# Kernel tuning notes

Hardware: AMD Instinct MI355X
Metric: run time of the kernel (lower is better)

Reference implementation:

```python
import jax, jax.numpy as jnp
import numpy as np

C = 64  # num_features

def setup_inputs() -> dict:
    key = jax.random.key(0)
    k = jax.random.split(key, 5)
    B, H, W = 4, 512, 512
    s = 1.0 / np.sqrt(C)
    return {
        "features": jax.random.normal(k[0], (B, C, H, W), jnp.float32),
        "w_ih": jax.random.uniform(k[1], (3 * C, 3 * C), jnp.float32, -s, s),
        "w_hh": jax.random.uniform(k[2], (3 * C, C), jnp.float32, -s, s),
        "b_ih": jax.random.uniform(k[3], (3 * C,), jnp.float32, -s, s),
        "b_hh": jax.random.uniform(k[4], (3 * C,), jnp.float32, -s, s),
    }

def _gru_cell(x, h, w_ih, w_hh, b_ih, b_hh):
    # PyTorch GRUCell: gates ordered [reset, update, new]
    gi = x @ w_ih.T + b_ih
    gh = h @ w_hh.T + b_hh
    i_r, i_z, i_n = jnp.split(gi, 3, axis=-1)
    h_r, h_z, h_n = jnp.split(gh, 3, axis=-1)
    r = jax.nn.sigmoid(i_r + h_r)
    z = jax.nn.sigmoid(i_z + h_z)
    n = jnp.tanh(i_n + r * h_n)
    return (1.0 - z) * n + z * h

def reference(features, w_ih, w_hh, b_ih, b_hh):
    B, Cf, H, W = features.shape
    # move scan axis (W) to front: [W, B, H, C]
    f = jnp.transpose(features, (3, 0, 2, 1))
    pad = jnp.zeros((B, 1, Cf), features.dtype)

    def step(prev_col, cur_col):
        # prev_col: already-updated column d-1, [B, H, C]
        nb = jnp.concatenate([pad, prev_col, pad], axis=1)  # [B, H+2, C]
        x = jnp.concatenate([nb[:, :-2], nb[:, 1:-1], nb[:, 2:]], axis=-1)  # [B, H, 3C]
        new = _gru_cell(x.reshape(B * H, 3 * Cf), cur_col.reshape(B * H, Cf),
                        w_ih, w_hh, b_ih, b_hh).reshape(B, H, Cf)
        return new, new

    col0 = f[0]
    _, outs = jax.lax.scan(step, col0, f[1:])
    all_cols = jnp.concatenate([col0[None], outs], axis=0)  # [W, B, H, C]
    return jnp.transpose(all_cols, (1, 3, 2, 0))  # [B, C, H, W]
```

## Files before the change

### kernel.cpp

```cpp
#include <hip/hip_runtime.h>

typedef short short8 __attribute__((ext_vector_type(8)));
typedef float f32x4 __attribute__((ext_vector_type(4)));
typedef unsigned short u16;
typedef unsigned int u32;

#define C64 64
#define HWp (512*512)
#define NWG 256
#define PR 72
#define SLOTS 18
#define SBUF 2048
#define UBUF 2048
#define NEP 128

struct Ws {
  int flags[NWG][32];
  u32 haloT[NWG][2][4*64];
  u32 haloB[NWG][2][4*64];
};

__device__ __forceinline__ u16 f2bf(float f){
  u32 r;
  asm("v_cvt_pk_bf16_f32 %0, %1, %1" : "=v"(r) : "v"(f));
  return (u16)r;
}
__device__ __forceinline__ float bf2f(u16 h){ return __uint_as_float(((u32)h) << 16); }
__device__ __forceinline__ f32x4 splat4(float x){ f32x4 v = {x,x,x,x}; return v; }
__device__ __forceinline__ float sigm(float x){ return 1.f/(1.f + __expf(-x)); }
__device__ __forceinline__ float tanh_(float x){ float e = __expf(2.f*x); return 1.f - 2.f/(e + 1.f); }

#define MFMA16(a,b,c) __builtin_amdgcn_mfma_f32_16x16x32_bf16(a,b,c,0,0,0)
#define ATOM_ST(p,v) __hip_atomic_store((p),(v),__ATOMIC_RELAXED,__HIP_MEMORY_SCOPE_AGENT)
#define ATOM_LD(p)   __hip_atomic_load((p),__ATOMIC_RELAXED,__HIP_MEMORY_SCOPE_AGENT)
#define DOT3(acc, XH, XL, WH, WL) \
  acc = MFMA16(XH, WH, acc); acc = MFMA16(XL, WH, acc); acc = MFMA16(XH, WL, acc);

__global__ void reset_flags(int* flags) {
  if (threadIdx.x < NWG) flags[threadIdx.x * 32] = -1;
}

#define AKK(kk) {                                                        \
  const int _o = PS + aoff + ((kk)>>1)*PR + ((kk)&1)*32;                 \
  short8 Ah = *(const short8*)&sh[_o];                                   \
  short8 Al = *(const short8*)&sl[_o];                                   \
  DOT3(aR, Ah, Al, BihH[0][kk], BihL[0][kk]);                            \
  DOT3(aZ, Ah, Al, BihH[1][kk], BihL[1][kk]);                            \
  DOT3(aI, Ah, Al, BihH[2][kk], BihL[2][kk]); }

#define XKT(kt) {                                                        \
  const int _o = PU + aoff + (kt)*32;                                    \
  short8 Xh = *(const short8*)&uh[_o];                                   \
  short8 Xl = *(const short8*)&ul[_o];                                   \
  DOT3(aR, Xh, Xl, BhhH[0][kt], BhhL[0][kt]);                            \
  DOT3(aZ, Xh, Xl, BhhH[1][kt], BhhL[1][kt]);                            \
  DOT3(aH, Xh, Xl, BhhH[2][kt], BhhL[2][kt]); }

#define GWB(j) {                                                         \
  const int m = kgrp*4 + (j);                                            \
  const int absr = a - 4 + m;                                            \
  float r = sigm(aR[j]);                                                 \
  float z = sigm(aZ[j]);                                                 \
  float nn = tanh_(aI[j] + r*aH[j]);                                     \
  float cur = bf2f(uh[PU + m*PR + ch]) + bf2f(ul[PU + m*PR + ch]);       \
  float v = (1.f - z)*nn + z*cur;                                        \
  if ((unsigned)absr < 512u) {                                           \
    u16 h_ = f2bf(v);                                                    \
    sh[PN + (m+1)*PR + ch] = h_;                                         \
    sl[PN + (m+1)*PR + ch] = f2bf(v - bf2f(h_));                         \
  }                                                                      \
  if (m >= 4 && m < 12) ost[((m-4)*64 + ch)*16 + dc0 + DD] = f2bf(v);    \
  if (DD == 3) {                                                         \
    if (kgrp == 1) ATOM_ST(&ws->haloT[g][e&1][(j)*64 + ch], __float_as_uint(v)); \
    if (kgrp == 2) ATOM_ST(&ws->haloB[g][e&1][(j)*64 + ch], __float_as_uint(v)); \
  } }

#define UST(i) {                                                         \
  float v = cv[DD][i];                                                   \
  u16 h_ = f2bf(v);                                                      \
  uh[PV + uoff[i]] = h_;                                                 \
  ul[PV + uoff[i]] = f2bf(v - bf2f(h_));                                 \
  cv[DD][i] = nv[i]; }

#define STEP(DD_) {                                                      \
  enum { DD = DD_, PS = (DD&1)*SBUF, PN = ((DD&1)^1)*SBUF,               \
         PU = (DD&1)*UBUF, PV = ((DD&1)^1)*UBUF };                       \
  float nv[4];                                                           \
  { int cc = 4*e + 6 + DD; if (cc > 511) cc = 511;                       \
    nv[0] = fval0 ? frow0[cc] : 0.f;                                     \
    nv[1] = fval1 ? frow1[cc] : 0.f;                                     \
    nv[2] = fval2 ? frow2[cc] : 0.f;                                     \
    nv[3] = fval3 ? frow3[cc] : 0.f; }                                   \
  f32x4 aR = splat4(biasR), aZ = splat4(biasZ);                          \
  f32x4 aI = splat4(biasI), aH = splat4(biasHn);                         \
  AKK(0) AKK(1) AKK(2) AKK(3) AKK(4) AKK(5)                              \
  XKT(0) XKT(1)                                                          \
  GWB(0) GWB(1) GWB(2) GWB(3)                                            \
  UST(0) UST(1) UST(2) UST(3)                                            \
}

__global__ __launch_bounds__(256, 1)
void gru_scan(const float* __restrict__ feat,
              const float* __restrict__ w_ih,
              const float* __restrict__ w_hh,
              const float* __restrict__ b_ih,
              const float* __restrict__ b_hh,
              float* __restrict__ out,
              Ws* __restrict__ ws)
{
  __shared__ __align__(16) u16 sh[2*SBUF], sl[2*SBUF];
  __shared__ __align__(16) u16 uh[2*UBUF], ul[2*UBUF];
  __shared__ __align__(16) u16 ost[8*64*16];

  const int tid  = threadIdx.x;
  const int wgid = blockIdx.x;
  const int g    = (wgid & 7) * 32 + (wgid >> 3);
  const int b    = g >> 6;
  const int kband= g & 63;
  const int a    = kband * 8;
  const int lane = tid & 63;
  const int wid  = tid >> 6;
  const int ln16 = lane & 15;
  const int kgrp = lane >> 4;
  const int ch   = wid*16 + ln16;

  short8 BihH[3][6], BihL[3][6], BhhH[3][2], BhhL[3][2];
#pragma unroll
  for (int gg = 0; gg < 3; ++gg) {
    const int n = gg*64 + ch;
#pragma unroll
    for (int kk = 0; kk < 6; ++kk) {
      short8 vh, vl;
#pragma unroll
      for (int j = 0; j < 8; ++j) {
        float wv = w_ih[n*192 + kk*32 + kgrp*8 + j];
        u16 h = f2bf(wv); vh[j] = (short)h; vl[j] = (short)f2bf(wv - bf2f(h));
      }
      BihH[gg][kk] = vh; BihL[gg][kk] = vl;
    }
#pragma unroll
    for (int kt = 0; kt < 2; ++kt) {
      short8 vh, vl;
#pragma unroll
      for (int j = 0; j < 8; ++j) {
        float wv = w_hh[n*64 + kt*32 + kgrp*8 + j];
        u16 h = f2bf(wv); vh[j] = (short)h; vl[j] = (short)f2bf(wv - bf2f(h));
      }
      BhhH[gg][kt] = vh; BhhL[gg][kt] = vl;
    }
  }
  const float biasR  = b_ih[ch]       + b_hh[ch];
  const float biasZ  = b_ih[64 + ch]  + b_hh[64 + ch];
  const float biasI  = b_ih[128 + ch];
  const float biasHn = b_hh[128 + ch];

  const int aoff = ln16*PR + kgrp*8;
  const int lch  = tid & 63;
  const int lr0  = wid * 4;
  int uoff[4];
#pragma unroll
  for (int i = 0; i < 4; ++i) uoff[i] = (lr0 + i)*PR + lch;

  const float* fbase = feat + (size_t)(b*C64 + lch)*HWp;
  int ar0 = a - 4 + lr0;
  const bool fval0 = (unsigned)(ar0+0) < 512u;
  const bool fval1 = (unsigned)(ar0+1) < 512u;
  const bool fval2 = (unsigned)(ar0+2) < 512u;
  const bool fval3 = (unsigned)(ar0+3) < 512u;
  const float* frow0 = fbase + (size_t)(fval0 ? ar0+0 : 0)*512;
  const float* frow1 = fbase + (size_t)(fval1 ? ar0+1 : 0)*512;
  const float* frow2 = fbase + (size_t)(fval2 ? ar0+2 : 0)*512;
  const float* frow3 = fbase + (size_t)(fval3 ? ar0+3 : 0)*512;

  for (int i = tid; i < 2*SBUF; i += 256) { sh[i] = 0; sl[i] = 0; }
  for (int i = tid; i < 2*UBUF; i += 256) { uh[i] = 0; ul[i] = 0; }
  __syncthreads();
#pragma unroll
  for (int i = 0; i < 5; ++i) {
    const int s = wid + 4*i;
    if (s < SLOTS) {
      const int absr = a - 5 + s;
      if ((unsigned)absr < 512u) {
        float v = fbase[(size_t)absr*512];
        u16 h_ = f2bf(v);
        sh[s*PR + lch] = h_;
        sl[s*PR + lch] = f2bf(v - bf2f(h_));
        if (s >= 5 && s <= 12) out[(size_t)(b*C64 + lch)*HWp + (size_t)absr*512] = v;
      }
    }
  }
  float cv[4][4];
#pragma unroll
  for (int i = 0; i < 4; ++i) {
    const int absr = a - 4 + lr0 + i;
    const bool val = (unsigned)absr < 512u;
    const float* fr = fbase + (size_t)(val ? absr : 0)*512;
    float v1 = val ? fr[1] : 0.f;
    u16 h_ = f2bf(v1);
    uh[uoff[i]] = h_;
    ul[uoff[i]] = f2bf(v1 - bf2f(h_));
    cv[0][i] = val ? fr[2] : 0.f;
    cv[1][i] = val ? fr[3] : 0.f;
    cv[2][i] = val ? fr[4] : 0.f;
    cv[3][i] = val ? fr[5] : 0.f;
  }
  __syncthreads();

#pragma unroll 1
  for (int e = 0; e < NEP; ++e) {
    const int dc0 = (e & 3) * 4;
    STEP(0)
    __syncthreads();
    STEP(1)
    __syncthreads();
    STEP(2)
    if (e < NEP-1) {
      __syncthreads();
      STEP(3)
    }

    asm volatile("s_waitcnt vmcnt(0)" ::: "memory");
    __syncthreads();
    if (e < NEP-1 && tid == 0) ATOM_ST(&ws->flags[g][0], e);

    if (wid == 0 || wid == 3) {
      if ((e & 3) == 3) {
        const int t128  = (wid == 0) ? lane : 64 + lane;
        const int wbase = 4*(e-3) + 1;
#pragma unroll
        for (int i = 0; i < 4; ++i) {
          const int pi  = t128 + 128*i;
          const int row = pi >> 6, c = pi & 63;
          float* go = out + (size_t)(b*C64 + c)*HWp + (size_t)(a + row)*512 + wbase;
#pragma unroll
          for (int dc = 0; dc < 16; ++dc)
            if (wbase + dc <= 511) go[dc] = bf2f(ost[pi*16 + dc]);
        }
      }
    } else if (e < NEP-1) {
      if (wid == 1 && kband > 0) {
        int f = -1, guard = 0;
        while (f < e && ++guard < (1<<17)) {
          if (lane == 0) f = ATOM_LD(&ws->flags[g-1][0]);
          f = __shfl(f, 0);
          if (f < e) __builtin_amdgcn_s_sleep(1);
        }
        asm volatile("" ::: "memory");
#pragma unroll
        for (int i = 0; i < 4; ++i) {
          float v = __uint_as_float(ATOM_LD(&ws->haloB[g-1][e&1][i*64 + lane]));
          u16 h_ = f2bf(v);
          sh[(1+i)*PR + lane] = h_;
          sl[(1+i)*PR + lane] = f2bf(v - bf2f(h_));
        }
      }
      if (wid == 2 && kband < 63) {
        int f = -1, guard = 0;
        while (f < e && ++guard < (1<<17)) {
          if (lane == 0) f = ATOM_LD(&ws->flags[g+1][0]);
          f = __shfl(f, 0);
          if (f < e) __builtin_amdgcn_s_sleep(1);
        }
        asm volatile("" ::: "memory");
#pragma unroll
        for (int i = 0; i < 4; ++i) {
          float v = __uint_as_float(ATOM_LD(&ws->haloT[g+1][e&1][i*64 + lane]));
          u16 h_ = f2bf(v);
          sh[(13+i)*PR + lane] = h_;
          sl[(13+i)*PR + lane] = f2bf(v - bf2f(h_));
        }
      }
    }
    __syncthreads();
  }
}

extern "C" void kernel_launch(void* const* d_in, const int* in_sizes, int n_in,
                              void* d_out, int out_size, void* d_ws, size_t ws_size,
                              hipStream_t stream) {
  const float* feat = (const float*)d_in[0];
  const float* wih  = (const float*)d_in[1];
  const float* whh  = (const float*)d_in[2];
  const float* bih  = (const float*)d_in[3];
  const float* bhh  = (const float*)d_in[4];
  float* out = (float*)d_out;
  Ws* ws = (Ws*)d_ws;

  reset_flags<<<1, NWG, 0, stream>>>((int*)ws->flags);
  gru_scan<<<NWG, 256, 0, stream>>>(feat, wih, whh, bih, bhh, out, ws);
}
```

Measured before the change: 1.278 ms.

## Split MFMA accumulator chains, batch feature prefetch, and remap cur-column ownership

Each gate's MFMA accumulation now runs as two independent chains that are summed at the end, which shortens the dependent MFMA latency chain. Feature loads for the next four columns are now issued once per epoch as vector loads instead of scalar loads inside each step. Lanes are remapped so the thread that writes the current-column values into LDS also holds them in a register for the gate update, removing the LDS reads of cur. The output staging buffer is transposed to column-major, which changes LDS bank patterns on write and readback. The cost is more accumulator registers and a larger live register set under a one-block-per-CU launch bound.

After: 1.420 ms. 11.1% more time.

```diff
diff --git a/kernel.cpp b/kernel.cpp
--- a/kernel.cpp
+++ b/kernel.cpp
@@ -2,6 +2,7 @@
 
 typedef short short8 __attribute__((ext_vector_type(8)));
 typedef float f32x4 __attribute__((ext_vector_type(4)));
+typedef float f32x2 __attribute__((ext_vector_type(2)));
 typedef unsigned short u16;
 typedef unsigned int u32;
 
@@ -40,36 +41,36 @@
   if (threadIdx.x < NWG) flags[threadIdx.x * 32] = -1;
 }
 
-#define AKK(kk) {                                                        \
+#define AKK(S, kk) {                                                     \
   const int _o = PS + aoff + ((kk)>>1)*PR + ((kk)&1)*32;                 \
   short8 Ah = *(const short8*)&sh[_o];                                   \
   short8 Al = *(const short8*)&sl[_o];                                   \
-  DOT3(aR, Ah, Al, BihH[0][kk], BihL[0][kk]);                            \
-  DOT3(aZ, Ah, Al, BihH[1][kk], BihL[1][kk]);                            \
-  DOT3(aI, Ah, Al, BihH[2][kk], BihL[2][kk]); }
-
-#define XKT(kt) {                                                        \
+  DOT3(aR##S, Ah, Al, BihH[0][kk], BihL[0][kk]);                         \
+  DOT3(aZ##S, Ah, Al, BihH[1][kk], BihL[1][kk]);                         \
+  DOT3(aI##S, Ah, Al, BihH[2][kk], BihL[2][kk]); }
+
+#define XKT(S, kt) {                                                     \
   const int _o = PU + aoff + (kt)*32;                                    \
   short8 Xh = *(const short8*)&uh[_o];                                   \
   short8 Xl = *(const short8*)&ul[_o];                                   \
-  DOT3(aR, Xh, Xl, BhhH[0][kt], BhhL[0][kt]);                            \
-  DOT3(aZ, Xh, Xl, BhhH[1][kt], BhhL[1][kt]);                            \
-  DOT3(aH, Xh, Xl, BhhH[2][kt], BhhL[2][kt]); }
+  DOT3(aR##S, Xh, Xl, BhhH[0][kt], BhhL[0][kt]);                         \
+  DOT3(aZ##S, Xh, Xl, BhhH[1][kt], BhhL[1][kt]);                         \
+  DOT3(aH##S, Xh, Xl, BhhH[2][kt], BhhL[2][kt]); }
 
 #define GWB(j) {                                                         \
   const int m = kgrp*4 + (j);                                            \
   const int absr = a - 4 + m;                                            \
-  float r = sigm(aR[j]);                                                 \
-  float z = sigm(aZ[j]);                                                 \
-  float nn = tanh_(aI[j] + r*aH[j]);                                     \
-  float cur = bf2f(uh[PU + m*PR + ch]) + bf2f(ul[PU + m*PR + ch]);       \
-  float v = (1.f - z)*nn + z*cur;                                        \
+  float r = sigm(aR0[j] + aR1[j]);                                       \
+  float z = sigm(aZ0[j] + aZ1[j]);                                       \
+  float nn = tanh_(aI0[j] + aI1[j] + r*(aH0[j] + aH1[j]));               \
+  float v = (1.f - z)*nn + z*cur[j];                                     \
   if ((unsigned)absr < 512u) {                                           \
     u16 h_ = f2bf(v);                                                    \
     sh[PN + (m+1)*PR + ch] = h_;                                         \
     sl[PN + (m+1)*PR + ch] = f2bf(v - bf2f(h_));                         \
   }                                                                      \
-  if (m >= 4 && m < 12) ost[((m-4)*64 + ch)*16 + dc0 + DD] = f2bf(v);    \
+  if (m >= 4 && m < 12)                                                  \
+    ost[(dc0 + DD)*512 + (m-4)*64 + ch] = f2bf(v);                       \
   if (DD == 3) {                                                         \
     if (kgrp == 1) ATOM_ST(&ws->haloT[g][e&1][(j)*64 + ch], __float_as_uint(v)); \
     if (kgrp == 2) ATOM_ST(&ws->haloB[g][e&1][(j)*64 + ch], __float_as_uint(v)); \
@@ -77,24 +78,21 @@
 
 #define UST(i) {                                                         \
   float v = cv[DD][i];                                                   \
+  cur[i] = v;                                                            \
   u16 h_ = f2bf(v);                                                      \
   uh[PV + uoff[i]] = h_;                                                 \
   ul[PV + uoff[i]] = f2bf(v - bf2f(h_));                                 \
-  cv[DD][i] = nv[i]; }
+  cv[DD][i] = nv4[i][DD]; }
 
 #define STEP(DD_) {                                                      \
   enum { DD = DD_, PS = (DD&1)*SBUF, PN = ((DD&1)^1)*SBUF,               \
          PU = (DD&1)*UBUF, PV = ((DD&1)^1)*UBUF };                       \
-  float nv[4];                                                           \
-  { int cc = 4*e + 6 + DD; if (cc > 511) cc = 511;                       \
-    nv[0] = fval0 ? frow0[cc] : 0.f;                                     \
-    nv[1] = fval1 ? frow1[cc] : 0.f;                                     \
-    nv[2] = fval2 ? frow2[cc] : 0.f;                                     \
-    nv[3] = fval3 ? frow3[cc] : 0.f; }                                   \
-  f32x4 aR = splat4(biasR), aZ = splat4(biasZ);                          \
-  f32x4 aI = splat4(biasI), aH = splat4(biasHn);                         \
-  AKK(0) AKK(1) AKK(2) AKK(3) AKK(4) AKK(5)                              \
-  XKT(0) XKT(1)                                                          \
+  f32x4 aR0 = splat4(biasR), aZ0 = splat4(biasZ);                        \
+  f32x4 aI0 = splat4(biasI), aH0 = splat4(biasHn);                       \
+  f32x4 aR1 = splat4(0.f), aZ1 = splat4(0.f);                            \
+  f32x4 aI1 = splat4(0.f), aH1 = splat4(0.f);                            \
+  AKK(0,0) AKK(1,3) AKK(0,1) AKK(1,4) AKK(0,2) AKK(1,5)                  \
+  XKT(0,0) XKT(1,1)                                                      \
   GWB(0) GWB(1) GWB(2) GWB(3)                                            \
   UST(0) UST(1) UST(2) UST(3)                                            \
 }
@@ -110,7 +108,7 @@
 {
   __shared__ __align__(16) u16 sh[2*SBUF], sl[2*SBUF];
   __shared__ __align__(16) u16 uh[2*UBUF], ul[2*UBUF];
-  __shared__ __align__(16) u16 ost[8*64*16];
+  __shared__ __align__(16) u16 ost[16*512];
 
   const int tid  = threadIdx.x;
   const int wgid = blockIdx.x;
@@ -155,60 +153,83 @@
   const float biasHn = b_hh[128 + ch];
 
   const int aoff = ln16*PR + kgrp*8;
-  const int lch  = tid & 63;
-  const int lr0  = wid * 4;
+  const int lrow = kgrp * 4;
   int uoff[4];
 #pragma unroll
-  for (int i = 0; i < 4; ++i) uoff[i] = (lr0 + i)*PR + lch;
-
-  const float* fbase = feat + (size_t)(b*C64 + lch)*HWp;
-  int ar0 = a - 4 + lr0;
-  const bool fval0 = (unsigned)(ar0+0) < 512u;
-  const bool fval1 = (unsigned)(ar0+1) < 512u;
-  const bool fval2 = (unsigned)(ar0+2) < 512u;
-  const bool fval3 = (unsigned)(ar0+3) < 512u;
-  const float* frow0 = fbase + (size_t)(fval0 ? ar0+0 : 0)*512;
-  const float* frow1 = fbase + (size_t)(fval1 ? ar0+1 : 0)*512;
-  const float* frow2 = fbase + (size_t)(fval2 ? ar0+2 : 0)*512;
-  const float* frow3 = fbase + (size_t)(fval3 ? ar0+3 : 0)*512;
+  for (int i = 0; i < 4; ++i) uoff[i] = (lrow + i)*PR + ch;
+
+  const float* fbase = feat + (size_t)(b*C64 + ch)*HWp;
+  const int ar0 = a - 4 + lrow;
+  bool fv[4];
+  const float* frw[4];
+#pragma unroll
+  for (int i = 0; i < 4; ++i) {
+    fv[i]  = (unsigned)(ar0 + i) < 512u;
+    frw[i] = fbase + (size_t)(fv[i] ? ar0 + i : 0)*512;
+  }
 
   for (int i = tid; i < 2*SBUF; i += 256) { sh[i] = 0; sl[i] = 0; }
   for (int i = tid; i < 2*UBUF; i += 256) { uh[i] = 0; ul[i] = 0; }
   __syncthreads();
-#pragma unroll
-  for (int i = 0; i < 5; ++i) {
-    const int s = wid + 4*i;
-    if (s < SLOTS) {
-      const int absr = a - 5 + s;
-      if ((unsigned)absr < 512u) {
-        float v = fbase[(size_t)absr*512];
-        u16 h_ = f2bf(v);
-        sh[s*PR + lch] = h_;
-        sl[s*PR + lch] = f2bf(v - bf2f(h_));
-        if (s >= 5 && s <= 12) out[(size_t)(b*C64 + lch)*HWp + (size_t)absr*512] = v;
-      }
-    }
-  }
-  float cv[4][4];
+  {
+    const int c0 = tid & 63;
+    const float* f0 = feat + (size_t)(b*C64 + c0)*HWp;
+#pragma unroll
+    for (int i = 0; i < 5; ++i) {
+      const int s = wid + 4*i;
+      if (s < SLOTS) {
+        const int absr = a - 5 + s;
+        if ((unsigned)absr < 512u) {
+          float v = f0[(size_t)absr*512];
+          u16 h_ = f2bf(v);
+          sh[s*PR + c0] = h_;
+          sl[s*PR + c0] = f2bf(v - bf2f(h_));
+          if (s >= 5 && s <= 12) out[(size_t)(b*C64 + c0)*HWp + (size_t)absr*512] = v;
+        }
+      }
+    }
+  }
+  float cv[4][4], cur[4], nv4[4][4];
 #pragma unroll
   for (int i = 0; i < 4; ++i) {
-    const int absr = a - 4 + lr0 + i;
-    const bool val = (unsigned)absr < 512u;
-    const float* fr = fbase + (size_t)(val ? absr : 0)*512;
-    float v1 = val ? fr[1] : 0.f;
+    float v1 = fv[i] ? frw[i][1] : 0.f;
     u16 h_ = f2bf(v1);
     uh[uoff[i]] = h_;
     ul[uoff[i]] = f2bf(v1 - bf2f(h_));
-    cv[0][i] = val ? fr[2] : 0.f;
-    cv[1][i] = val ? fr[3] : 0.f;
-    cv[2][i] = val ? fr[4] : 0.f;
-    cv[3][i] = val ? fr[5] : 0.f;
+    cur[i]   = v1;
+    cv[0][i] = fv[i] ? frw[i][2] : 0.f;
+    cv[1][i] = fv[i] ? frw[i][3] : 0.f;
+    cv[2][i] = fv[i] ? frw[i][4] : 0.f;
+    cv[3][i] = fv[i] ? frw[i][5] : 0.f;
   }
   __syncthreads();
 
 #pragma unroll 1
   for (int e = 0; e < NEP; ++e) {
     const int dc0 = (e & 3) * 4;
+    {
+      const int cc = 4*e + 6;
+      if (cc + 3 <= 511) {
+#pragma unroll
+        for (int i = 0; i < 4; ++i) {
+          f32x2 p = *(const f32x2*)&frw[i][cc];
+          f32x2 q = *(const f32x2*)&frw[i][cc + 2];
+          nv4[i][0] = fv[i] ? p[0] : 0.f;
+          nv4[i][1] = fv[i] ? p[1] : 0.f;
+          nv4[i][2] = fv[i] ? q[0] : 0.f;
+          nv4[i][3] = fv[i] ? q[1] : 0.f;
+        }
+      } else {
+#pragma unroll
+        for (int i = 0; i < 4; ++i)
+#pragma unroll
+          for (int d = 0; d < 4; ++d) {
+            int c2 = cc + d; if (c2 > 511) c2 = 511;
+            nv4[i][d] = fv[i] ? frw[i][c2] : 0.f;
+          }
+      }
+    }
+
     STEP(0)
     __syncthreads();
     STEP(1)
@@ -234,7 +255,7 @@
           float* go = out + (size_t)(b*C64 + c)*HWp + (size_t)(a + row)*512 + wbase;
 #pragma unroll
           for (int dc = 0; dc < 16; ++dc)
-            if (wbase + dc <= 511) go[dc] = bf2f(ost[pi*16 + dc]);
+            if (wbase + dc <= 511) go[dc] = bf2f(ost[dc*512 + row*64 + c]);
         }
       }
     } else if (e < NEP-1) {
```
